# Performance work log

Hardware: AMD Instinct MI355X
Metric: run time of the kernel (lower is better)

Reference implementation:

```python
import jax, jax.numpy as jnp
import numpy as np

B, P, C = 8, 16384, 5          # images, proposals/img, classes (incl. background)
K = 100                         # detections_per_img (greedy-NMS iterations)
SCORE_THRESH = 0.05
NMS_THRESH = 0.5
W_XY, W_WH = 10.0, 5.0          # bbox_reg_weights (10,10,5,5)
BBOX_XFORM_CLIP = float(np.log(1000.0 / 16.0))
NEG = jnp.float32(-1e30)


def setup_inputs() -> dict:
    key = jax.random.key(0)
    ks = jax.random.split(key, 8)
    N = B * P
    class_logits = jax.random.normal(ks[0], (N, C), jnp.float32)
    box_regression = jax.random.normal(ks[1], (N, C * 4), jnp.float32) * 0.1
    handside_logits = jax.random.normal(ks[2], (N, C), jnp.float32)
    dxdymag_logits = jax.random.normal(ks[3], (N, C * 3), jnp.float32)
    contact_logits = jax.random.normal(ks[4], (N, C * 5), jnp.float32)
    # valid proposal boxes x1<x2, y1<y2 inside an ~800x1216 image
    x1 = jax.random.uniform(ks[5], (B, P), jnp.float32) * 1100.0
    y1 = jax.random.uniform(ks[6], (B, P), jnp.float32) * 700.0
    wh = jax.random.uniform(ks[7], (B, P, 2), jnp.float32) * 100.0 + 4.0
    proposals = jnp.stack([x1, y1, x1 + wh[..., 0], y1 + wh[..., 1]], axis=-1)
    image_hw = jnp.array([800, 1216], jnp.int32)
    return dict(class_logits=class_logits, box_regression=box_regression,
                handside_logits=handside_logits, dxdymag_logits=dxdymag_logits,
                contact_logits=contact_logits, proposals=proposals, image_hw=image_hw)


def _decode(rel, props):
    # rel [N,C,4], props [N,4] -> [N,C,4] (torchvision BoxCoder.decode)
    w = props[:, 2] - props[:, 0]
    h = props[:, 3] - props[:, 1]
    cx = props[:, 0] + 0.5 * w
    cy = props[:, 1] + 0.5 * h
    dx = rel[..., 0] / W_XY
    dy = rel[..., 1] / W_XY
    dw = jnp.minimum(rel[..., 2] / W_WH, BBOX_XFORM_CLIP)
    dh = jnp.minimum(rel[..., 3] / W_WH, BBOX_XFORM_CLIP)
    pcx = dx * w[:, None] + cx[:, None]
    pcy = dy * h[:, None] + cy[:, None]
    pw = jnp.exp(dw) * w[:, None]
    ph = jnp.exp(dh) * h[:, None]
    return jnp.stack([pcx - 0.5 * pw, pcy - 0.5 * ph,
                      pcx + 0.5 * pw, pcy + 0.5 * ph], axis=-1)


def _iou_one_vs_all(box, boxes):
    lt = jnp.maximum(box[:2], boxes[:, :2])
    rb = jnp.minimum(box[2:], boxes[:, 2:])
    whd = jnp.clip(rb - lt, 0.0)
    inter = whd[:, 0] * whd[:, 1]
    a1 = (box[2] - box[0]) * (box[3] - box[1])
    a2 = (boxes[:, 2] - boxes[:, 0]) * (boxes[:, 3] - boxes[:, 1])
    return inter / (a1 + a2 - inter)


def _nms_image(boxes, scores, labels):
    # class-aware greedy NMS (batched_nms coordinate-offset trick), fixed K iters.
    off = labels.astype(boxes.dtype) * (jax.lax.stop_gradient(boxes).max() + 1.0)
    obox = jax.lax.stop_gradient(boxes) + off[:, None]

    def step(s, _):
        i = jnp.argmax(s)
        keep = s[i] > NEG * 0.5
        iou = _iou_one_vs_all(obox[i], obox)
        s = jnp.where((iou > NMS_THRESH) & keep, NEG, s)
        s = s.at[i].set(NEG)
        return s, (i, keep)

    _, (idx, keep) = jax.lax.scan(step, scores, None, length=K)
    return idx, keep


def reference(class_logits, box_regression, handside_logits, dxdymag_logits,
              contact_logits, proposals, image_hw):
    N = class_logits.shape[0]
    pred_boxes = _decode(box_regression.reshape(N, C, 4), proposals.reshape(-1, 4))
    pred_scores = jax.nn.softmax(class_logits, axis=-1)          # [N,C]
    pred_sides = (jax.nn.sigmoid(handside_logits) > 0.5).astype(jnp.float32)
    pred_dxdy = dxdymag_logits.reshape(N, C, 3)
    pred_contacts = jnp.argmax(contact_logits.reshape(N, C, 5), axis=2)
    # clip boxes to image (image_shape = (H, W))
    Hh = image_hw[0].astype(jnp.float32)
    Ww = image_hw[1].astype(jnp.float32)
    xs = jnp.clip(pred_boxes[..., 0::2], 0.0, Ww)
    ys = jnp.clip(pred_boxes[..., 1::2], 0.0, Hh)
    pred_boxes = jnp.stack([xs[..., 0], ys[..., 0], xs[..., 1], ys[..., 1]], -1)
    # drop background class, flatten per image (class-fastest order, as torch reshape)
    Cm1 = C - 1
    boxes = pred_boxes[:, 1:].reshape(B, P * Cm1, 4)
    scores = pred_scores[:, 1:].reshape(B, P * Cm1)
    sides = pred_sides[:, 1:].reshape(B, P * Cm1)
    dxdy = pred_dxdy[:, 1:].reshape(B, P * Cm1, 3)
    contacts = pred_contacts[:, 1:].reshape(B, P * Cm1)
    labels = jnp.broadcast_to(jnp.tile(jnp.arange(1, C), P), (B, P * Cm1))
    # score thresholding via masking (scores <= thresh never selected)
    ms = jnp.where(scores > SCORE_THRESH, scores, NEG)
    idx, keep = jax.vmap(_nms_image)(boxes, ms, labels)          # [B,K]
    kf = keep.astype(jnp.float32)
    out_boxes = jnp.take_along_axis(boxes, idx[:, :, None], 1) * kf[:, :, None]
    out_scores = jnp.take_along_axis(scores, idx, 1) * kf
    out_labels = jnp.where(keep, jnp.take_along_axis(labels, idx, 1), 0)
    out_sides = jnp.take_along_axis(sides, idx, 1) * kf
    out_dxdy = jnp.take_along_axis(dxdy, idx[:, :, None], 1) * kf[:, :, None]
    out_contacts = jnp.where(keep, jnp.take_along_axis(contacts, idx, 1), 0)
    return (out_boxes, out_scores, out_labels, out_sides, out_dxdy, out_contacts, keep)
```

## Files before the change

kernel.cpp:

```cpp
#include <hip/hip_runtime.h>
#include <cstdint>

typedef unsigned int u32;
typedef unsigned long long u64;

constexpr int B_ = 8;
constexpr int P_ = 16384;
constexpr int K_ = 100;
constexpr int M_ = P_ * 4;
constexpr int TSEL = 192;
constexpr int CAP = 256;
constexpr int NBP = 576;
constexpr u32 BASE16 = 0x3D4Cu;
constexpr float SCORE_T = 0.05f;
constexpr float CLIPV = 4.135166556742356f;

__device__ inline int aphys(int i) {
  return (i < CAP) ? ((((i & 63) + ((i >> 6) << 2)) & 63) | (i & 192)) : i;
}

__global__ __launch_bounds__(256) void prep_kernel(
    const float* __restrict__ logits,
    const float* __restrict__ boxreg,
    const float* __restrict__ props,
    const int*  __restrict__ image_hw,
    float* __restrict__ wboxes,
    float* __restrict__ wscores,
    float* __restrict__ wblockmax,
    u32*   __restrict__ bhist)
{
  __shared__ u32 lh[NBP];
  __shared__ float red[256];
  for (int i = threadIdx.x; i < NBP; i += 256) lh[i] = 0u;
  __syncthreads();

  const int n = blockIdx.x * 256 + threadIdx.x;

  float l[5];
#pragma unroll
  for (int i = 0; i < 5; ++i) l[i] = logits[n * 5 + i];
  float mx = l[0];
#pragma unroll
  for (int i = 1; i < 5; ++i) mx = fmaxf(mx, l[i]);
  float e[5]; float ssum = 0.f;
#pragma unroll
  for (int i = 0; i < 5; ++i) { e[i] = expf(l[i] - mx); ssum += e[i]; }

  const float4 pr = reinterpret_cast<const float4*>(props)[n];
  const float w  = pr.z - pr.x;
  const float h  = pr.w - pr.y;
  const float cx = pr.x + 0.5f * w;
  const float cy = pr.y + 0.5f * h;
  const float Hf = (float)image_hw[0];
  const float Wf = (float)image_hw[1];

  float bmax = 0.f;
  float sc[4];
#pragma unroll
  for (int c = 1; c < 5; ++c) {
    const float4 rel = reinterpret_cast<const float4*>(boxreg)[n * 5 + c];
    const float dx = rel.x / 10.0f;
    const float dy = rel.y / 10.0f;
    const float dw = fminf(rel.z / 5.0f, CLIPV);
    const float dh = fminf(rel.w / 5.0f, CLIPV);
    const float pcx = dx * w + cx;
    const float pcy = dy * h + cy;
    const float pw = expf(dw) * w;
    const float ph = expf(dh) * h;
    float x1 = pcx - 0.5f * pw, y1 = pcy - 0.5f * ph;
    float x2 = pcx + 0.5f * pw, y2 = pcy + 0.5f * ph;
    x1 = fminf(fmaxf(x1, 0.f), Wf);
    x2 = fminf(fmaxf(x2, 0.f), Wf);
    y1 = fminf(fmaxf(y1, 0.f), Hf);
    y2 = fminf(fmaxf(y2, 0.f), Hf);
    reinterpret_cast<float4*>(wboxes)[n * 4 + (c - 1)] = make_float4(x1, y1, x2, y2);
    bmax = fmaxf(bmax, fmaxf(fmaxf(x1, x2), fmaxf(y1, y2)));
    const float sv = e[c] / ssum;
    sc[c - 1] = sv;
    if (sv > SCORE_T) {
      u32 bin = (__float_as_uint(sv) >> 16) - BASE16;
      if (bin >= (u32)NBP) bin = NBP - 1;
      atomicAdd(&lh[bin], 1u);
    }
  }
  reinterpret_cast<float4*>(wscores)[n] = make_float4(sc[0], sc[1], sc[2], sc[3]);

  __syncthreads();
  for (int i = threadIdx.x; i < NBP; i += 256)
    bhist[(size_t)blockIdx.x * NBP + i] = lh[i];

  red[threadIdx.x] = bmax;
  __syncthreads();
#pragma unroll
  for (int off = 128; off > 0; off >>= 1) {
    if (threadIdx.x < off) red[threadIdx.x] = fmaxf(red[threadIdx.x], red[threadIdx.x + off]);
    __syncthreads();
  }
  if (threadIdx.x == 0) wblockmax[blockIdx.x] = red[0];
}

__global__ __launch_bounds__(512) void thresh_kernel(
    const u32* __restrict__ bhist, u32* __restrict__ Xthr, int* __restrict__ Carr,
    int* __restrict__ remv, int* __restrict__ offs)
{
  const int b = blockIdx.x, t = threadIdx.x;
  __shared__ u32 agg[NBP];
  __shared__ u32 X_s;
  __shared__ int binX_s, C_sh, rem_sh;
  __shared__ int sg[64];

  for (int bin = t; bin < NBP; bin += 512) {
    u32 s = 0;
    const u32* h = bhist + (size_t)(b * 64) * NBP + bin;
    for (int g = 0; g < 64; ++g) s += h[(size_t)g * NBP];
    agg[bin] = s;
  }
  __syncthreads();

  if (t < 64) {
    const int lo = NBP - t * 9 - 9;
    u32 hb[9]; int mysum = 0;
#pragma unroll
    for (int q = 0; q < 9; ++q) { hb[q] = agg[lo + q]; mysum += (int)hb[q]; }
    int inc = mysum;
#pragma unroll
    for (int off = 1; off < 64; off <<= 1) {
      const int v = __shfl_up(inc, off);
      if (t >= off) inc += v;
    }
    const int tot = __shfl(inc, 63);
    const int pre = inc - mysum;
    if (tot < TSEL) {
      if (t == 63) { X_s = BASE16 << 16; binX_s = 0; C_sh = tot; rem_sh = 0; }
    } else if (pre < TSEL && inc >= TSEL) {
      int cum = pre, kb = lo, qsel = 8;
      for (int q = 8; q >= 0; --q) {
        cum += (int)hb[q];
        if (cum >= TSEL) { kb = lo + q; qsel = q; break; }
      }
      int C = cum;
      u32 Xbin;
      if (C > CAP) { C -= (int)hb[qsel]; Xbin = (u32)(kb + 1); }
      else Xbin = (u32)kb;
      X_s = (BASE16 + Xbin) << 16;
      binX_s = (int)Xbin; C_sh = C; rem_sh = tot - C;
    }
  }
  __syncthreads();
  const int binX = binX_s;

  {
    const int g = t >> 3, lsub = t & 7;
    const u32* h = bhist + (size_t)(b * 64 + g) * NBP;
    int cg = 0;
    for (int bin = binX + lsub; bin < NBP; bin += 8) cg += (int)h[bin];
#pragma unroll
    for (int off = 1; off < 8; off <<= 1) cg += __shfl_xor(cg, off);
    if (lsub == 0) sg[g] = cg;
  }
  __syncthreads();
  if (t < 64) {
    const int v = sg[t];
    int inc = v;
#pragma unroll
    for (int off = 1; off < 64; off <<= 1) {
      const int u = __shfl_up(inc, off);
      if (t >= off) inc += u;
    }
    offs[b * 64 + t] = inc - v;
  }
  if (t == 0) { Xthr[b] = X_s; Carr[b] = C_sh; remv[b] = rem_sh; }
}

__global__ __launch_bounds__(256) void compact_kernel(
    const float* __restrict__ wscores, const u32* __restrict__ Xthr,
    const int* __restrict__ offs, u64* __restrict__ keybuf)
{
  const int blk = blockIdx.x;
  const int b = blk >> 6;
  const int n = blk * 256 + threadIdx.x;
  const u32 X = Xthr[b];
  __shared__ int cnt;
  if (threadIdx.x == 0) cnt = 0;
  __syncthreads();
  const int base = b * CAP + offs[blk];

  const float4 v = reinterpret_cast<const float4*>(wscores)[n];
  const float ss[4] = {v.x, v.y, v.z, v.w};
  const int j0 = (n & (P_ - 1)) * 4;
#pragma unroll
  for (int c = 0; c < 4; ++c) {
    if (ss[c] > SCORE_T) {
      const u32 bb = __float_as_uint(ss[c]);
      if (bb >= X) {
        const int pos = atomicAdd(&cnt, 1);
        keybuf[base + pos] = ((u64)bb << 16) | (u64)(65535 - (j0 + c));
      }
    }
  }
}

__global__ __launch_bounds__(512) void nms_kernel(
    const float* __restrict__ wboxes, const float* __restrict__ wscores,
    const float* __restrict__ wblockmax, const u32* __restrict__ Xthr,
    const int* __restrict__ remv, const int* __restrict__ Carr,
    const u64* __restrict__ keybuf,
    const float* __restrict__ handside, const float* __restrict__ dxdymag,
    const float* __restrict__ contact, float* __restrict__ out)
{
  const int b = blockIdx.x, t = threadIdx.x;
  const float4* boxes4 = reinterpret_cast<const float4*>(wboxes);
  const float4* sc4 = reinterpret_cast<const float4*>(wscores) + (size_t)b * (M_ / 4);
  const u32 X = Xthr[b];

  __shared__ float maxv_s;
  __shared__ u64   kall[CAP];
  __shared__ u64   skey[CAP];
  __shared__ float4 cb4[CAP + K_];
  __shared__ float carea[CAP + K_];
  __shared__ float cscf[CAP + K_];
  __shared__ int   cj[CAP + K_];
  __shared__ u64   supmask[CAP * 4];
  __shared__ u64   km[4];
  __shared__ int   chg;
  __shared__ int   kidx[K_];
  __shared__ int   kcount_s, nslow_s;
  __shared__ u64   red2[512];
  __shared__ u64   bitmap[1024];

  if (t < 64) {
    float v = wblockmax[b * 64 + t];
#pragma unroll
    for (int off = 32; off > 0; off >>= 1) v = fmaxf(v, __shfl_xor(v, off));
    if (t == 0) maxv_s = v;
  }
  if (t == 0) { kcount_s = 0; nslow_s = 0; }
  const int C = min(Carr[b], CAP);
  if (t < CAP) kall[t] = (t < C) ? keybuf[b * CAP + t] : 0ull;
  __syncthreads();
  const float maxv1 = maxv_s + 1.0f;

  if (t < CAP) {
    const u64 my = kall[t];
    u32 r = 0;
    for (int u = 0; u < CAP; ++u) r += (kall[u] > my) ? 1u : 0u;
    if (t < C) skey[r] = my;
  }
  __syncthreads();

  if (t < C) {
    const u64 key = skey[t];
    const int j = 65535 - (int)(key & 0xFFFFull);
    const int cls = (j & 3) + 1;
    const float4 bx = boxes4[(size_t)b * M_ + j];
    const float offv = (float)cls * maxv1;
    const float ox1 = bx.x + offv, oy1 = bx.y + offv;
    const float ox2 = bx.z + offv, oy2 = bx.w + offv;
    const int ph = aphys(t);
    cb4[ph] = make_float4(ox1, oy1, ox2, oy2);
    carea[ph] = (ox2 - ox1) * (oy2 - oy1);
    cscf[ph] = __uint_as_float((u32)(key >> 16));
    cj[ph] = j;
  }
  __syncthreads();

  for (int task = t; task < C * 4; task += 512) {
    const int i = task >> 2, wq = task & 3;
    const float4 ib = cb4[aphys(i)];
    const float ia = carea[aphys(i)];
    u64 m = 0;
    const int qb = wq * 64, qe = min(qb + 64, C);
    for (int q = qb; q < qe; ++q) {
      if (q == i) continue;
      const int qp = aphys(q);
      const float4 qbx = cb4[qp];
      const float ltx = fmaxf(ib.x, qbx.x);
      const float lty = fmaxf(ib.y, qbx.y);
      const float rbx = fminf(ib.z, qbx.z);
      const float rby = fminf(ib.w, qbx.w);
      const float iw = fmaxf(rbx - ltx, 0.f);
      const float ih = fmaxf(rby - lty, 0.f);
      const float inter = iw * ih;
      const float iou = inter / (ia + carea[qp] - inter);
      if (iou > 0.5f) m |= 1ull << (q - qb);
    }
    supmask[i * 4 + wq] = m;
  }
  __syncthreads();

  const int wi = t >> 6, bi = t & 63;
  const u64 lowmask = bi ? (~0ull >> (64 - bi)) : 0ull;
  u64 rb0 = 0, rb1 = 0, rb2 = 0, rb3 = 0;
  const bool alive = (t < C);
  if (t < CAP) {
    rb0 = supmask[t * 4 + 0];
    rb1 = supmask[t * 4 + 1];
    rb2 = supmask[t * 4 + 2];
    rb3 = supmask[t * 4 + 3];
    const u64 m0 = (wi > 0) ? ~0ull : lowmask;
    const u64 m1 = (wi > 1) ? ~0ull : ((wi == 1) ? lowmask : 0ull);
    const u64 m2 = (wi > 2) ? ~0ull : ((wi == 2) ? lowmask : 0ull);
    const u64 m3 = (wi == 3) ? lowmask : 0ull;
    rb0 &= m0; rb1 &= m1; rb2 &= m2; rb3 &= m3;
    const u64 bal = __ballot(alive ? 1 : 0);
    if (bi == 0) km[wi] = bal;
  }
  __syncthreads();
  while (true) {
    if (t == 0) chg = 0;
    __syncthreads();
    u64 nb = 0;
    if (t < CAP) {
      const u64 k0 = km[0], k1 = km[1], k2 = km[2], k3 = km[3];
      const bool sup = ((rb0 & k0) | (rb1 & k1) | (rb2 & k2) | (rb3 & k3)) != 0ull;
      const bool kn = alive && !sup;
      nb = __ballot(kn ? 1 : 0);
      if (bi == 0 && nb != km[wi]) chg = 1;
    }
    __syncthreads();
    if (t < CAP && bi == 0) km[wi] = nb;
    __syncthreads();
    if (!chg) break;
  }

  if (t < CAP) {
    const u64 kw = km[wi];
    if ((kw >> bi) & 1ull) {
      int pb = 0;
      if (wi > 0) pb += __popcll(km[0]);
      if (wi > 1) pb += __popcll(km[1]);
      if (wi > 2) pb += __popcll(km[2]);
      pb += __popcll(kw & lowmask);
      if (pb < K_) kidx[pb] = t;
    }
    if (t == 0) {
      kcount_s = min(__popcll(km[0]) + __popcll(km[1]) +
                     __popcll(km[2]) + __popcll(km[3]), K_);
    }
  }
  __syncthreads();

  if (kcount_s < K_ && remv[b] > 0) {
    for (int i = t; i < 1024; i += 512) bitmap[i] = 0ull;
    __syncthreads();
    while (true) {
      u64 best = 0ull;
      for (int i = t; i < M_ / 4; i += 512) {
        const float4 v = sc4[i];
        const float ss[4] = {v.x, v.y, v.z, v.w};
#pragma unroll
        for (int c = 0; c < 4; ++c) {
          if (ss[c] > SCORE_T) {
            const u32 bb = __float_as_uint(ss[c]);
            if (bb < X) {
              const int j = i * 4 + c;
              if (!((bitmap[j >> 6] >> (j & 63)) & 1ull)) {
                const u64 key = ((u64)bb << 16) | (u64)(65535 - j);
                if (key > best) best = key;
              }
            }
          }
        }
      }
      red2[t] = best;
      __syncthreads();
      for (int off = 256; off > 0; off >>= 1) {
        if (t < off && red2[t + off] > red2[t]) red2[t] = red2[t + off];
        __syncthreads();
      }
      const u64 wkey = red2[0];
      if (wkey == 0ull) break;
      if (t == 0) {
        const int j = 65535 - (int)(wkey & 0xFFFFull);
        bitmap[j >> 6] |= 1ull << (j & 63);
        const int cls = (j & 3) + 1;
        const float4 bx = boxes4[(size_t)b * M_ + j];
        const float offv = (float)cls * maxv1;
        const float ox1 = bx.x + offv, oy1 = bx.y + offv;
        const float ox2 = bx.z + offv, oy2 = bx.w + offv;
        const float ar = (ox2 - ox1) * (oy2 - oy1);
        bool sup = false;
        for (int k2 = 0; k2 < kcount_s; ++k2) {
          const int ki = aphys(kidx[k2]);
          const float4 kb = cb4[ki];
          const float ltx = fmaxf(kb.x, ox1);
          const float lty = fmaxf(kb.y, oy1);
          const float rbx = fminf(kb.z, ox2);
          const float rby = fminf(kb.w, oy2);
          const float iw = fmaxf(rbx - ltx, 0.f);
          const float ih = fmaxf(rby - lty, 0.f);
          const float inter = iw * ih;
          const float iou = inter / (carea[ki] + ar - inter);
          if (iou > 0.5f) { sup = true; break; }
        }
        if (!sup) {
          const int slot = CAP + nslow_s;
          cb4[slot] = make_float4(ox1, oy1, ox2, oy2);
          carea[slot] = ar;
          cscf[slot] = __uint_as_float((u32)(wkey >> 16));
          cj[slot] = j;
          kidx[kcount_s] = slot;
          ++nslow_s;
          ++kcount_s;
        }
      }
      __syncthreads();
      if (kcount_s >= K_) break;
    }
    __syncthreads();
  }
  __syncthreads();

  const int kc = kcount_s;
  if (t < K_) {
    const int r = t;
    float ob0 = 0.f, ob1 = 0.f, ob2 = 0.f, ob3 = 0.f;
    float osc = 0.f, olab = 0.f, oside = 0.f;
    float od0 = 0.f, od1 = 0.f, od2 = 0.f;
    float ocon = 0.f, okeep = 0.f;
    if (r < kc) {
      const int idx = kidx[r];
      const int ph = aphys(idx);
      const int j = cj[ph];
      const int cls = (j & 3) + 1;
      const int n = b * P_ + (j >> 2);
      const float4 bx = boxes4[(size_t)b * M_ + j];
      ob0 = bx.x; ob1 = bx.y; ob2 = bx.z; ob3 = bx.w;
      osc = cscf[ph];
      olab = (float)cls;
      oside = (handside[n * 5 + cls] > 0.f) ? 1.f : 0.f;
      od0 = dxdymag[n * 15 + cls * 3 + 0];
      od1 = dxdymag[n * 15 + cls * 3 + 1];
      od2 = dxdymag[n * 15 + cls * 3 + 2];
      float bvv = contact[n * 25 + cls * 5 + 0];
      int best = 0;
#pragma unroll
      for (int i = 1; i < 5; ++i) {
        const float ci = contact[n * 25 + cls * 5 + i];
        if (ci > bvv) { bvv = ci; best = i; }
      }
      ocon = (float)best;
      okeep = 1.f;
    }
    const int gb = b * K_ + r;
    out[gb * 4 + 0] = ob0;
    out[gb * 4 + 1] = ob1;
    out[gb * 4 + 2] = ob2;
    out[gb * 4 + 3] = ob3;
    out[3200 + gb] = osc;
    out[4000 + gb] = olab;
    out[4800 + gb] = oside;
    out[5600 + gb * 3 + 0] = od0;
    out[5600 + gb * 3 + 1] = od1;
    out[5600 + gb * 3 + 2] = od2;
    out[8000 + gb] = ocon;
    out[8800 + gb] = okeep;
  }
}

extern "C" void kernel_launch(void* const* d_in, const int* in_sizes, int n_in,
                              void* d_out, int out_size, void* d_ws, size_t ws_size,
                              hipStream_t stream) {
  const float* class_logits = (const float*)d_in[0];
  const float* box_reg      = (const float*)d_in[1];
  const float* handside     = (const float*)d_in[2];
  const float* dxdymag      = (const float*)d_in[3];
  const float* contact      = (const float*)d_in[4];
  const float* proposals    = (const float*)d_in[5];
  const int*   image_hw     = (const int*)d_in[6];
  float* out = (float*)d_out;

  char* ws = (char*)d_ws;
  u32*   bhist     = (u32*)  ws;
  u32*   Xthr      = (u32*)  (ws + 1179648);
  int*   Carr      = (int*)  (ws + 1179680);
  int*   remv      = (int*)  (ws + 1179712);
  int*   offs      = (int*)  (ws + 1179776);
  float* wblockmax = (float*)(ws + 1181824);
  u64*   keybuf    = (u64*)  (ws + 1183872);
  float* wscores   = (float*)(ws + 2097152);
  float* wboxes    = (float*)(ws + 4194304);

  prep_kernel<<<dim3(512), dim3(256), 0, stream>>>(
      class_logits, box_reg, proposals, image_hw, wboxes, wscores, wblockmax, bhist);
  thresh_kernel<<<dim3(B_), dim3(512), 0, stream>>>(bhist, Xthr, Carr, remv, offs);
  compact_kernel<<<dim3(512), dim3(256), 0, stream>>>(wscores, Xthr, offs, keybuf);
  nms_kernel<<<dim3(B_), dim3(512), 0, stream>>>(
      wboxes, wscores, wblockmax, Xthr, remv, Carr, keybuf,
      handside, dxdymag, contact, out);
}
```

Before: 53.19 us.

## Drop decoded box buffer, decode candidates on demand, use global atomic compaction

The prep kernel no longer writes all decoded boxes (8 MB) to workspace. The NMS kernel instead recomputes the decode for the few selected candidates from box_regression and proposals, and keeps the decoded boxes in shared memory for the output stage. The threshold kernel drops its per-block prefix-offset pass and builds the histogram with coalesced reads plus shared atomics. Compaction now uses one global atomic counter per image with a CAP guard, which makes keybuf order nondeterministic and adds atomic contention in exchange for fewer passes.

```diff
diff --git a/kernel.cpp b/kernel.cpp
--- a/kernel.cpp
+++ b/kernel.cpp
@@ -19,12 +19,33 @@
   return (i < CAP) ? ((((i & 63) + ((i >> 6) << 2)) & 63) | (i & 192)) : i;
 }
 
+__device__ inline float4 decode_clip(float4 rel, float4 pr, float Wf, float Hf) {
+  const float w  = pr.z - pr.x;
+  const float h  = pr.w - pr.y;
+  const float cx = pr.x + 0.5f * w;
+  const float cy = pr.y + 0.5f * h;
+  const float dx = rel.x / 10.0f;
+  const float dy = rel.y / 10.0f;
+  const float dw = fminf(rel.z / 5.0f, CLIPV);
+  const float dh = fminf(rel.w / 5.0f, CLIPV);
+  const float pcx = dx * w + cx;
+  const float pcy = dy * h + cy;
+  const float pw = expf(dw) * w;
+  const float ph = expf(dh) * h;
+  float x1 = pcx - 0.5f * pw, y1 = pcy - 0.5f * ph;
+  float x2 = pcx + 0.5f * pw, y2 = pcy + 0.5f * ph;
+  x1 = fminf(fmaxf(x1, 0.f), Wf);
+  x2 = fminf(fmaxf(x2, 0.f), Wf);
+  y1 = fminf(fmaxf(y1, 0.f), Hf);
+  y2 = fminf(fmaxf(y2, 0.f), Hf);
+  return make_float4(x1, y1, x2, y2);
+}
+
 __global__ __launch_bounds__(256) void prep_kernel(
     const float* __restrict__ logits,
     const float* __restrict__ boxreg,
     const float* __restrict__ props,
     const int*  __restrict__ image_hw,
-    float* __restrict__ wboxes,
     float* __restrict__ wscores,
     float* __restrict__ wblockmax,
     u32*   __restrict__ bhist)
@@ -47,10 +68,6 @@
   for (int i = 0; i < 5; ++i) { e[i] = expf(l[i] - mx); ssum += e[i]; }
 
   const float4 pr = reinterpret_cast<const float4*>(props)[n];
-  const float w  = pr.z - pr.x;
-  const float h  = pr.w - pr.y;
-  const float cx = pr.x + 0.5f * w;
-  const float cy = pr.y + 0.5f * h;
   const float Hf = (float)image_hw[0];
   const float Wf = (float)image_hw[1];
 
@@ -59,22 +76,8 @@
 #pragma unroll
   for (int c = 1; c < 5; ++c) {
     const float4 rel = reinterpret_cast<const float4*>(boxreg)[n * 5 + c];
-    const float dx = rel.x / 10.0f;
-    const float dy = rel.y / 10.0f;
-    const float dw = fminf(rel.z / 5.0f, CLIPV);
-    const float dh = fminf(rel.w / 5.0f, CLIPV);
-    const float pcx = dx * w + cx;
-    const float pcy = dy * h + cy;
-    const float pw = expf(dw) * w;
-    const float ph = expf(dh) * h;
-    float x1 = pcx - 0.5f * pw, y1 = pcy - 0.5f * ph;
-    float x2 = pcx + 0.5f * pw, y2 = pcy + 0.5f * ph;
-    x1 = fminf(fmaxf(x1, 0.f), Wf);
-    x2 = fminf(fmaxf(x2, 0.f), Wf);
-    y1 = fminf(fmaxf(y1, 0.f), Hf);
-    y2 = fminf(fmaxf(y2, 0.f), Hf);
-    reinterpret_cast<float4*>(wboxes)[n * 4 + (c - 1)] = make_float4(x1, y1, x2, y2);
-    bmax = fmaxf(bmax, fmaxf(fmaxf(x1, x2), fmaxf(y1, y2)));
+    const float4 bx = decode_clip(rel, pr, Wf, Hf);
+    bmax = fmaxf(bmax, fmaxf(fmaxf(bx.x, bx.z), fmaxf(bx.y, bx.w)));
     const float sv = e[c] / ssum;
     sc[c - 1] = sv;
     if (sv > SCORE_T) {
@@ -101,19 +104,20 @@
 
 __global__ __launch_bounds__(512) void thresh_kernel(
     const u32* __restrict__ bhist, u32* __restrict__ Xthr, int* __restrict__ Carr,
-    int* __restrict__ remv, int* __restrict__ offs)
+    int* __restrict__ remv, int* __restrict__ selcnt)
 {
   const int b = blockIdx.x, t = threadIdx.x;
   __shared__ u32 agg[NBP];
   __shared__ u32 X_s;
-  __shared__ int binX_s, C_sh, rem_sh;
-  __shared__ int sg[64];
-
-  for (int bin = t; bin < NBP; bin += 512) {
-    u32 s = 0;
-    const u32* h = bhist + (size_t)(b * 64) * NBP + bin;
-    for (int g = 0; g < 64; ++g) s += h[(size_t)g * NBP];
-    agg[bin] = s;
+  __shared__ int C_sh, rem_sh;
+
+  for (int i = t; i < NBP; i += 512) agg[i] = 0u;
+  __syncthreads();
+
+  const u32* src = bhist + (size_t)(b * 64) * NBP;
+  for (int idx = t; idx < 64 * NBP; idx += 512) {
+    const u32 v = src[idx];
+    if (v) atomicAdd(&agg[idx % NBP], v);
   }
   __syncthreads();
 
@@ -131,7 +135,7 @@
     const int tot = __shfl(inc, 63);
     const int pre = inc - mysum;
     if (tot < TSEL) {
-      if (t == 63) { X_s = BASE16 << 16; binX_s = 0; C_sh = tot; rem_sh = 0; }
+      if (t == 63) { X_s = BASE16 << 16; C_sh = tot; rem_sh = 0; }
     } else if (pre < TSEL && inc >= TSEL) {
       int cum = pre, kb = lo, qsel = 8;
       for (int q = 8; q >= 0; --q) {
@@ -143,48 +147,20 @@
       if (C > CAP) { C -= (int)hb[qsel]; Xbin = (u32)(kb + 1); }
       else Xbin = (u32)kb;
       X_s = (BASE16 + Xbin) << 16;
-      binX_s = (int)Xbin; C_sh = C; rem_sh = tot - C;
-    }
-  }
-  __syncthreads();
-  const int binX = binX_s;
-
-  {
-    const int g = t >> 3, lsub = t & 7;
-    const u32* h = bhist + (size_t)(b * 64 + g) * NBP;
-    int cg = 0;
-    for (int bin = binX + lsub; bin < NBP; bin += 8) cg += (int)h[bin];
-#pragma unroll
-    for (int off = 1; off < 8; off <<= 1) cg += __shfl_xor(cg, off);
-    if (lsub == 0) sg[g] = cg;
-  }
-  __syncthreads();
-  if (t < 64) {
-    const int v = sg[t];
-    int inc = v;
-#pragma unroll
-    for (int off = 1; off < 64; off <<= 1) {
-      const int u = __shfl_up(inc, off);
-      if (t >= off) inc += u;
-    }
-    offs[b * 64 + t] = inc - v;
-  }
-  if (t == 0) { Xthr[b] = X_s; Carr[b] = C_sh; remv[b] = rem_sh; }
+      C_sh = C; rem_sh = tot - C;
+    }
+  }
+  __syncthreads();
+  if (t == 0) { Xthr[b] = X_s; Carr[b] = C_sh; remv[b] = rem_sh; selcnt[b] = 0; }
 }
 
 __global__ __launch_bounds__(256) void compact_kernel(
     const float* __restrict__ wscores, const u32* __restrict__ Xthr,
-    const int* __restrict__ offs, u64* __restrict__ keybuf)
+    int* __restrict__ selcnt, u64* __restrict__ keybuf)
 {
-  const int blk = blockIdx.x;
-  const int b = blk >> 6;
-  const int n = blk * 256 + threadIdx.x;
+  const int n = blockIdx.x * 256 + threadIdx.x;
+  const int b = n >> 14;
   const u32 X = Xthr[b];
-  __shared__ int cnt;
-  if (threadIdx.x == 0) cnt = 0;
-  __syncthreads();
-  const int base = b * CAP + offs[blk];
-
   const float4 v = reinterpret_cast<const float4*>(wscores)[n];
   const float ss[4] = {v.x, v.y, v.z, v.w};
   const int j0 = (n & (P_ - 1)) * 4;
@@ -193,30 +169,33 @@
     if (ss[c] > SCORE_T) {
       const u32 bb = __float_as_uint(ss[c]);
       if (bb >= X) {
-        const int pos = atomicAdd(&cnt, 1);
-        keybuf[base + pos] = ((u64)bb << 16) | (u64)(65535 - (j0 + c));
+        const int pos = atomicAdd(&selcnt[b], 1);
+        if (pos < CAP) keybuf[b * CAP + pos] = ((u64)bb << 16) | (u64)(65535 - (j0 + c));
       }
     }
   }
 }
 
 __global__ __launch_bounds__(512) void nms_kernel(
-    const float* __restrict__ wboxes, const float* __restrict__ wscores,
-    const float* __restrict__ wblockmax, const u32* __restrict__ Xthr,
-    const int* __restrict__ remv, const int* __restrict__ Carr,
-    const u64* __restrict__ keybuf,
+    const float* __restrict__ boxreg, const float* __restrict__ props,
+    const int* __restrict__ image_hw,
+    const float* __restrict__ wscores, const float* __restrict__ wblockmax,
+    const u32* __restrict__ Xthr, const int* __restrict__ remv,
+    const int* __restrict__ Carr, const u64* __restrict__ keybuf,
     const float* __restrict__ handside, const float* __restrict__ dxdymag,
     const float* __restrict__ contact, float* __restrict__ out)
 {
   const int b = blockIdx.x, t = threadIdx.x;
-  const float4* boxes4 = reinterpret_cast<const float4*>(wboxes);
   const float4* sc4 = reinterpret_cast<const float4*>(wscores) + (size_t)b * (M_ / 4);
   const u32 X = Xthr[b];
+  const float Hf = (float)image_hw[0];
+  const float Wf = (float)image_hw[1];
 
   __shared__ float maxv_s;
   __shared__ u64   kall[CAP];
   __shared__ u64   skey[CAP];
   __shared__ float4 cb4[CAP + K_];
+  __shared__ float4 cbx[CAP + K_];
   __shared__ float carea[CAP + K_];
   __shared__ float cscf[CAP + K_];
   __shared__ int   cj[CAP + K_];
@@ -252,12 +231,16 @@
     const u64 key = skey[t];
     const int j = 65535 - (int)(key & 0xFFFFull);
     const int cls = (j & 3) + 1;
-    const float4 bx = boxes4[(size_t)b * M_ + j];
+    const int n = b * P_ + (j >> 2);
+    const float4 rel = reinterpret_cast<const float4*>(boxreg)[n * 5 + cls];
+    const float4 pr  = reinterpret_cast<const float4*>(props)[n];
+    const float4 bx = decode_clip(rel, pr, Wf, Hf);
     const float offv = (float)cls * maxv1;
     const float ox1 = bx.x + offv, oy1 = bx.y + offv;
     const float ox2 = bx.z + offv, oy2 = bx.w + offv;
     const int ph = aphys(t);
     cb4[ph] = make_float4(ox1, oy1, ox2, oy2);
+    cbx[ph] = bx;
     carea[ph] = (ox2 - ox1) * (oy2 - oy1);
     cscf[ph] = __uint_as_float((u32)(key >> 16));
     cj[ph] = j;
@@ -374,7 +357,10 @@
         const int j = 65535 - (int)(wkey & 0xFFFFull);
         bitmap[j >> 6] |= 1ull << (j & 63);
         const int cls = (j & 3) + 1;
-        const float4 bx = boxes4[(size_t)b * M_ + j];
+        const int n = b * P_ + (j >> 2);
+        const float4 rel = reinterpret_cast<const float4*>(boxreg)[n * 5 + cls];
+        const float4 pr  = reinterpret_cast<const float4*>(props)[n];
+        const float4 bx = decode_clip(rel, pr, Wf, Hf);
         const float offv = (float)cls * maxv1;
         const float ox1 = bx.x + offv, oy1 = bx.y + offv;
         const float ox2 = bx.z + offv, oy2 = bx.w + offv;
@@ -396,6 +382,7 @@
         if (!sup) {
           const int slot = CAP + nslow_s;
           cb4[slot] = make_float4(ox1, oy1, ox2, oy2);
+          cbx[slot] = bx;
           carea[slot] = ar;
           cscf[slot] = __uint_as_float((u32)(wkey >> 16));
           cj[slot] = j;
@@ -424,7 +411,7 @@
       const int j = cj[ph];
       const int cls = (j & 3) + 1;
       const int n = b * P_ + (j >> 2);
-      const float4 bx = boxes4[(size_t)b * M_ + j];
+      const float4 bx = cbx[ph];
       ob0 = bx.x; ob1 = bx.y; ob2 = bx.z; ob3 = bx.w;
       osc = cscf[ph];
       olab = (float)cls;
@@ -475,17 +462,18 @@
   u32*   Xthr      = (u32*)  (ws + 1179648);
   int*   Carr      = (int*)  (ws + 1179680);
   int*   remv      = (int*)  (ws + 1179712);
-  int*   offs      = (int*)  (ws + 1179776);
+  int*   selcnt    = (int*)  (ws + 1179744);
   float* wblockmax = (float*)(ws + 1181824);
   u64*   keybuf    = (u64*)  (ws + 1183872);
   float* wscores   = (float*)(ws + 2097152);
-  float* wboxes    = (float*)(ws + 4194304);
 
   prep_kernel<<<dim3(512), dim3(256), 0, stream>>>(
-      class_logits, box_reg, proposals, image_hw, wboxes, wscores, wblockmax, bhist);
-  thresh_kernel<<<dim3(B_), dim3(512), 0, stream>>>(bhist, Xthr, Carr, remv, offs);
-  compact_kernel<<<dim3(512), dim3(256), 0, stream>>>(wscores, Xthr, offs, keybuf);
+      class_logits, box_reg, proposals, image_hw, wscores, wblockmax, bhist);
+  thresh_kernel<<<dim3(B_), dim3(512), 0, stream>>>(
+      bhist, Xthr, Carr, remv, selcnt);
+  compact_kernel<<<dim3(512), dim3(256), 0, stream>>>(
+      wscores, Xthr, selcnt, keybuf);
   nms_kernel<<<dim3(B_), dim3(512), 0, stream>>>(
-      wboxes, wscores, wblockmax, Xthr, remv, Carr, keybuf,
-      handside, dxdymag, contact, out);
-}
+      box_reg, proposals, image_hw, wscores, wblockmax, Xthr, remv, Carr,
+      keybuf, handside, dxdymag, contact, out);
+}
```

After: 86.05 us. +61.8%, slower.
